# Performance work log

Hardware: AMD Instinct MI355X
Metric: run time of the kernel (lower is better)

## Reference

```python
import jax, jax.numpy as jnp
import numpy as np

# MoELoRA dims
B, S, D = 4, 4096, 1024          # batch, seq, in_features
OUT = 3072                       # out_features (merged qkv)
R, E, G = 8, 8, 2                # lora rank, num experts, num enabled groups (q,v)
OD = OUT // 3                    # out channels per group
SCALING = 16.0 / 8.0             # lora_alpha / r


def setup_inputs() -> dict:
    key = jax.random.key(0)
    k0, k1, k2, k3 = jax.random.split(key, 4)
    x = jax.random.normal(k0, (B, S, D), dtype=jnp.float32)
    # routing linear weight [E, D] (nn.Linear stores [out, in])
    W_route = jax.random.normal(k1, (E, D), dtype=jnp.float32) * 0.02
    # per-expert lora_A reshaped to [E, G, R, D] (rows are group-major: G blocks of R)
    A = jax.random.normal(k2, (E, G, R, D), dtype=jnp.float32) * 0.02
    # per-expert lora_B reshaped to [E, G, OD, R] (grouped conv1d weight, kernel=1)
    Bw = jax.random.normal(k3, (E, G, OD, R), dtype=jnp.float32) * 0.02
    # enabled output columns: groups 0 (q) and 2 (v) of the 3-way split
    lora_ind = jnp.concatenate([jnp.arange(OD), jnp.arange(2 * OD, 3 * OD)]).astype(jnp.int64)
    return {"x": x, "W_route": W_route, "A": A, "Bw": Bw, "lora_ind": lora_ind}


def reference(x, W_route, A, Bw, lora_ind):
    # route_weight = softmax(x @ W_route^T) over experts  -> [B,S,E]
    route = jax.nn.softmax(jnp.einsum("bsd,ed->bse", x, W_route), axis=-1)
    # per-expert down-projection: F.linear(x, lora_A)  -> [B,S,E,G,R]
    h = jnp.einsum("bsd,egrd->bsegr", x, A)
    # route weighting commutes with the (linear) up-projection; weight h first
    # to avoid materializing the [B,S,E,G,OD] per-expert outputs.
    wh = h * route[..., None, None]                      # [B,S,E,G,R]
    # grouped conv1d (kernel=1) == per-group matmul; sum over experts
    compact = jnp.einsum("bsegr,egor->bsgo", wh, Bw) * SCALING   # [B,S,G,OD]
    compact = compact.reshape(B, S, G * OD)
    # zero_pad: scatter compact channels into enabled output columns
    out = jnp.zeros((B, S, OUT), dtype=compact.dtype).at[..., lora_ind].set(compact)
    return out
```

## Files before the change

### kernel.cpp

```cpp
#include <hip/hip_runtime.h>
#include <math.h>

#define NTOK   16384
#define DDIM   1024
#define NE     8
#define NF     128
#define FP     144
#define ODIM   1024
#define NOUT   3072
#define SCALE  2.0f
#define TOKB   32

typedef __attribute__((ext_vector_type(8))) short bf16x8;
typedef __attribute__((ext_vector_type(4))) float f32x4;

#define WS_ABT 0
#define WS_BBT 294912

__device__ inline unsigned f2bf(float a, float b) {
    union { float f; unsigned u; } ua, ub;
    ua.f = a; ub.f = b;
    unsigned x = ua.u + (0x7fffu + ((ua.u >> 16) & 1));
    unsigned y = ub.u + (0x7fffu + ((ub.u >> 16) & 1));
    return (x >> 16) | (y & 0xffff0000u);
}

__global__ __launch_bounds__(256) void k_prep(const float* __restrict__ A,
                                              const float* __restrict__ Wr,
                                              const float* __restrict__ Bw,
                                              unsigned short* __restrict__ Abt,
                                              unsigned short* __restrict__ Bbt) {
    const int b = blockIdx.x, t = threadIdx.x;
    if (b < FP) {
        const int col = t * 4;
        float4 v = {0.f, 0.f, 0.f, 0.f};
        if (b < NF)           v = *(const float4*)(A + (size_t)b * DDIM + col);
        else if (b < NF + NE) v = *(const float4*)(Wr + (size_t)(b - NF) * DDIM + col);
        uint2 p; p.x = f2bf(v.x, v.y); p.y = f2bf(v.z, v.w);
        *(uint2*)(Abt + (size_t)b * DDIM + col) = p;
    } else {
        const int idx = (b - FP) * 1024 + t * 4;
        const int g = idx >> 16, o = (idx >> 6) & 1023, er = idx & 63;
        const int e = er >> 3, r0 = er & 7;
        float4 v = *(const float4*)(Bw + ((size_t)(e * 2 + g) * ODIM + o) * 8 + r0);
        uint2 p; p.x = f2bf(v.x, v.y); p.y = f2bf(v.z, v.w);
        *(uint2*)(Bbt + idx) = p;
    }
}

__global__ __launch_bounds__(256) void k_fused(const float* __restrict__ x,
                                               const unsigned short* __restrict__ Abt,
                                               const unsigned short* __restrict__ Bbt,
                                               float* __restrict__ out) {
    __shared__ __align__(16) char smem[67584];
    unsigned short* xs = (unsigned short*)smem;
    unsigned short* ab = (unsigned short*)(smem + 12288);
    float* whs = (float*)smem;

    const int t    = threadIdx.x;
    const int tokb = blockIdx.x * TOKB;
    const int lane = t & 63, w = t >> 6;
    const int m    = w >> 1, h = w & 1;
    const int l15  = lane & 15, lq = lane >> 4;

    f32x4 acc[5];
#pragma unroll
    for (int n = 0; n < 5; ++n) acc[n] = (f32x4){0.f, 0.f, 0.f, 0.f};

    const int xtok = t >> 3;
    const int xc   = t & 7;
    float4 xr[3][2];

    auto LDX = [&](int set, int k0) {
        xr[set][0] = *(const float4*)(x + (size_t)(tokb + xtok) * DDIM + k0 + xc * 8);
        xr[set][1] = *(const float4*)(x + (size_t)(tokb + xtok) * DDIM + k0 + xc * 8 + 4);
    };
    auto WRX = [&](int j) {
        unsigned short* xb = xs + j * (TOKB * 64);
        uint4 p;
        p.x = f2bf(xr[j][0].x, xr[j][0].y); p.y = f2bf(xr[j][0].z, xr[j][0].w);
        p.z = f2bf(xr[j][1].x, xr[j][1].y); p.w = f2bf(xr[j][1].z, xr[j][1].w);
        const int c8 = xc ^ (xtok & 7);
        *(uint4*)(xb + xtok * 64 + c8 * 8) = p;
    };
    auto LDA = [&](int buf, int k0) {
        unsigned short* base = ab + buf * (144 * 64);
#pragma unroll
        for (int i = 0; i < 5; ++i) {
            if (i < 4 || t < 128) {
                const int c   = i * 256 + t;
                const int row = c >> 3;
                const int c8  = (c & 7) ^ (row & 7);
                const unsigned short* gp = Abt + (size_t)row * DDIM + k0 + c8 * 8;
                unsigned short* lp = base + (i * 256 + w * 64) * 8;
                __builtin_amdgcn_global_load_lds(
                    (const __attribute__((address_space(1))) unsigned int*)gp,
                    (__attribute__((address_space(3))) unsigned int*)lp, 16, 0, 0);
            }
        }
    };

    LDX(0, 0);   LDA(0, 0);
    LDX(1, 64);  LDA(1, 64);
    WRX(0);

#pragma unroll 16
    for (int s = 0; s < 16; ++s) {
        if (s == 15)    asm volatile("s_waitcnt vmcnt(0)" ::: "memory");
        else if (w < 2) asm volatile("s_waitcnt vmcnt(7)" ::: "memory");
        else            asm volatile("s_waitcnt vmcnt(6)" ::: "memory");
        asm volatile("s_waitcnt lgkmcnt(0)" ::: "memory");
        __builtin_amdgcn_sched_barrier(0);
        __builtin_amdgcn_s_barrier();
        __builtin_amdgcn_sched_barrier(0);
        if (s + 2 < 16) { LDX((s + 2) % 3, (s + 2) * 64); LDA((s + 2) % 3, (s + 2) * 64); }
        __builtin_amdgcn_sched_barrier(0);
        const unsigned short* xb  = xs + (s % 3) * (TOKB * 64);
        const unsigned short* abc = ab + (s % 3) * (144 * 64);
        __builtin_amdgcn_s_setprio(1);
#pragma unroll
        for (int ks = 0; ks < 2; ++ks) {
            const int sw = (((ks << 2) | lq) ^ (l15 & 7)) * 8;
            bf16x8 af = *(const bf16x8*)(xb + (m * 16 + l15) * 64 + sw);
#pragma unroll
            for (int j = 0; j < 4; ++j) {
                const int nt = 2 * j + h;
                bf16x8 bf = *(const bf16x8*)(abc + (nt * 16 + l15) * 64 + sw);
                acc[j] = __builtin_amdgcn_mfma_f32_16x16x32_bf16(af, bf, acc[j], 0, 0, 0);
            }
            bf16x8 bl = *(const bf16x8*)(abc + (8 * 16 + l15) * 64 + sw);
            acc[4] = __builtin_amdgcn_mfma_f32_16x16x32_bf16(af, bl, acc[4], 0, 0, 0);
        }
        __builtin_amdgcn_s_setprio(0);
        if (s + 1 < 16) WRX((s + 1) % 3);
    }

    float mx[4], pv[4], sm[4], rt[4];
#pragma unroll
    for (int r = 0; r < 4; ++r) mx[r] = acc[4][r];
#pragma unroll
    for (int msk = 1; msk <= 4; msk <<= 1)
#pragma unroll
        for (int r = 0; r < 4; ++r) mx[r] = fmaxf(mx[r], __shfl_xor(mx[r], msk, 16));
#pragma unroll
    for (int r = 0; r < 4; ++r) { pv[r] = expf(acc[4][r] - mx[r]); sm[r] = pv[r]; }
#pragma unroll
    for (int msk = 1; msk <= 4; msk <<= 1)
#pragma unroll
        for (int r = 0; r < 4; ++r) sm[r] += __shfl_xor(sm[r], msk, 16);
#pragma unroll
    for (int r = 0; r < 4; ++r) rt[r] = SCALE * pv[r] / sm[r];

    __syncthreads();

#pragma unroll
    for (int j = 0; j < 4; ++j) {
        const int e = 2 * j + h;
        float rb[4];
#pragma unroll
        for (int r = 0; r < 4; ++r) rb[r] = __shfl(rt[r], e, 16);
#pragma unroll
        for (int r = 0; r < 4; ++r)
            whs[(m * 16 + lq * 4 + r) * 140 + e * 16 + l15] = acc[j][r] * rb[r];
    }
    __syncthreads();

    bf16x8 paf[2];
#pragma unroll
    for (int ks = 0; ks < 2; ++ks) {
        const float* hp = whs + (m * 16 + l15) * 140 + ((ks << 2) | lq) * 16 + (h << 3);
        f32x4 v0 = *(const f32x4*)hp;
        f32x4 v1 = *(const f32x4*)(hp + 4);
        uint4 pk;
        pk.x = f2bf(v0[0], v0[1]); pk.y = f2bf(v0[2], v0[3]);
        pk.z = f2bf(v1[0], v1[1]); pk.w = f2bf(v1[2], v1[3]);
        paf[ks] = *(bf16x8*)&pk;
    }
    __syncthreads();

    float* tile = (float*)smem + w * (16 * 132);
    const int erow  = lane >> 5;
    const int ec4   = lane & 31;
    const int gcolb = h << 11;
    const int zcolb = 1024 + (h << 9);
    const float4 zf4 = {0.f, 0.f, 0.f, 0.f};
#pragma unroll 1
    for (int cb = 0; cb < 8; ++cb) {
#pragma unroll
        for (int nn = 0; nn < 8; ++nn) {
            const int n = cb * 8 + nn;
            const unsigned short* bp =
                Bbt + ((size_t)(h << 10) + (n << 4) + l15) * 64 + (lq << 3);
            bf16x8 b0 = *(const bf16x8*)bp;
            bf16x8 b1 = *(const bf16x8*)(bp + 32);
            f32x4 c = {0.f, 0.f, 0.f, 0.f};
            c = __builtin_amdgcn_mfma_f32_16x16x32_bf16(paf[0], b0, c, 0, 0, 0);
            c = __builtin_amdgcn_mfma_f32_16x16x32_bf16(paf[1], b1, c, 0, 0, 0);
#pragma unroll
            for (int r = 0; r < 4; ++r)
                tile[(lq * 4 + r) * 132 + nn * 16 + l15] = c[r];
        }
#pragma unroll
        for (int j = 0; j < 8; ++j) {
            const int row = j * 2 + erow;
            float4 v = *(const float4*)&tile[row * 132 + ec4 * 4];
            *(float4*)(out + (size_t)(tokb + m * 16 + row) * NOUT
                       + gcolb + cb * 128 + ec4 * 4) = v;
        }
#pragma unroll
        for (int i = 0; i < 4; ++i) {
            const int local = i * 64 + lane;
            const int row = cb * 2 + (local >> 7);
            const int c4  = local & 127;
            *(float4*)(out + (size_t)(tokb + m * 16 + row) * NOUT
                       + zcolb + c4 * 4) = zf4;
        }
    }
}

extern "C" void kernel_launch(void* const* d_in, const int* in_sizes, int n_in,
                              void* d_out, int out_size, void* d_ws, size_t ws_size,
                              hipStream_t stream) {
    const float* x  = (const float*)d_in[0];
    const float* Wr = (const float*)d_in[1];
    const float* A  = (const float*)d_in[2];
    const float* Bw = (const float*)d_in[3];
    unsigned short* Abt = (unsigned short*)((char*)d_ws + WS_ABT);
    unsigned short* Bbt = (unsigned short*)((char*)d_ws + WS_BBT);
    float* out = (float*)d_out;

    k_prep <<<FP + 128, 256, 0, stream>>>(A, Wr, Bw, Abt, Bbt);
    k_fused<<<NTOK / TOKB, 256, 0, stream>>>(x, Abt, Bbt, out);
}
```

Before: 62.53 us.

## Split fused kernel into separate down-projection and up-projection kernels

Splits the single fused kernel into two. The first computes the routed down-projection and writes bf16 weighted activations to a workspace buffer. The second reads those activations and runs the up-projection MFMA plus the output writes. The intent is for each kernel to use fewer resources (the up kernel needs less shared memory) and get better occupancy on the write-heavy output phase. The cost is an extra global round-trip for the intermediate (16384x128 bf16) and an extra launch.

```diff
diff --git a/kernel.cpp b/kernel.cpp
--- a/kernel.cpp
+++ b/kernel.cpp
@@ -16,6 +16,7 @@
 
 #define WS_ABT 0
 #define WS_BBT 294912
+#define WS_WH  557056
 
 __device__ inline unsigned f2bf(float a, float b) {
     union { float f; unsigned u; } ua, ub;
@@ -48,10 +49,9 @@
     }
 }
 
-__global__ __launch_bounds__(256) void k_fused(const float* __restrict__ x,
+__global__ __launch_bounds__(256) void k1_down(const float* __restrict__ x,
                                                const unsigned short* __restrict__ Abt,
-                                               const unsigned short* __restrict__ Bbt,
-                                               float* __restrict__ out) {
+                                               unsigned short* __restrict__ wh) {
     __shared__ __align__(16) char smem[67584];
     unsigned short* xs = (unsigned short*)smem;
     unsigned short* ab = (unsigned short*)(smem + 12288);
@@ -165,20 +165,38 @@
     }
     __syncthreads();
 
+    {
+        const int wtok = t >> 3, wc = (t & 7) * 16;
+        const float* hp = whs + wtok * 140 + wc;
+        uint4 q0, q1;
+        q0.x = f2bf(hp[0], hp[1]);   q0.y = f2bf(hp[2], hp[3]);
+        q0.z = f2bf(hp[4], hp[5]);   q0.w = f2bf(hp[6], hp[7]);
+        q1.x = f2bf(hp[8], hp[9]);   q1.y = f2bf(hp[10], hp[11]);
+        q1.z = f2bf(hp[12], hp[13]); q1.w = f2bf(hp[14], hp[15]);
+        unsigned short* wp = wh + (size_t)(tokb + wtok) * NF + wc;
+        *(uint4*)(wp) = q0;
+        *(uint4*)(wp + 8) = q1;
+    }
+}
+
+__global__ __launch_bounds__(256) void k2_up(const unsigned short* __restrict__ wh,
+                                             const unsigned short* __restrict__ Bbt,
+                                             float* __restrict__ out) {
+    __shared__ __align__(16) float tiles[4][16 * 132];
+
+    const int t    = threadIdx.x;
+    const int tokb = blockIdx.x * TOKB;
+    const int lane = t & 63, w = t >> 6;
+    const int m    = w >> 1, h = w & 1;
+    const int l15  = lane & 15, lq = lane >> 4;
+
     bf16x8 paf[2];
 #pragma unroll
-    for (int ks = 0; ks < 2; ++ks) {
-        const float* hp = whs + (m * 16 + l15) * 140 + ((ks << 2) | lq) * 16 + (h << 3);
-        f32x4 v0 = *(const f32x4*)hp;
-        f32x4 v1 = *(const f32x4*)(hp + 4);
-        uint4 pk;
-        pk.x = f2bf(v0[0], v0[1]); pk.y = f2bf(v0[2], v0[3]);
-        pk.z = f2bf(v1[0], v1[1]); pk.w = f2bf(v1[2], v1[3]);
-        paf[ks] = *(bf16x8*)&pk;
-    }
-    __syncthreads();
-
-    float* tile = (float*)smem + w * (16 * 132);
+    for (int ks = 0; ks < 2; ++ks)
+        paf[ks] = *(const bf16x8*)(wh + (size_t)(tokb + m * 16 + l15) * NF
+                                   + (((ks << 2) | lq) << 4) + (h << 3));
+
+    float* tile = tiles[w];
     const int erow  = lane >> 5;
     const int ec4   = lane & 31;
     const int gcolb = h << 11;
@@ -227,8 +245,10 @@
     const float* Bw = (const float*)d_in[3];
     unsigned short* Abt = (unsigned short*)((char*)d_ws + WS_ABT);
     unsigned short* Bbt = (unsigned short*)((char*)d_ws + WS_BBT);
+    unsigned short* wh  = (unsigned short*)((char*)d_ws + WS_WH);
     float* out = (float*)d_out;
 
     k_prep <<<FP + 128, 256, 0, stream>>>(A, Wr, Bw, Abt, Bbt);
-    k_fused<<<NTOK / TOKB, 256, 0, stream>>>(x, Abt, Bbt, out);
-}
+    k1_down<<<NTOK / TOKB, 256, 0, stream>>>(x, Abt, wh);
+    k2_up  <<<NTOK / TOKB, 256, 0, stream>>>(wh, Bbt, out);
+}
```

Measured after the change: 69.29 us. 1.11x slower.
